# Kernel optimization log

Hardware: AMD Instinct MI355X
Metric: run time of the kernel (lower is better)

The kernel has to match this reference:

```python
import jax, jax.numpy as jnp
import numpy as np

N = 100_000            # particles
E = 3_200_000          # edges (avg degree 32)
DIM = 3
H = 1.0                # kernel_radius
SIGMA = 3.0 / 359.0 / np.pi / H**3   # 3D quintic kernel normalization
RHO_REF = 1.0
P_REF = 100.0          # rho_ref * (10*u_ref)**2 / gamma, gamma=1
P_BG = 0.0             # p_bg_factor * p_ref
ETA0 = 0.01            # base_viscosity
EPS = 1e-8


def _qpows(d, p):
    q = d / H
    return (jnp.maximum(0.0, 1.0 - q) ** p,
            jnp.maximum(0.0, 2.0 - q) ** p,
            jnp.maximum(0.0, 3.0 - q) ** p)


def kernel_w(d):
    q1, q2, q3 = _qpows(d, 5)
    return SIGMA * (q3 - 6.0 * q2 + 15.0 * q1)


def kernel_grad_w(d):
    q1, q2, q3 = _qpows(d, 4)
    return (SIGMA / H) * (-5.0 * q3 + 30.0 * q2 - 75.0 * q1)


def setup_inputs() -> dict:
    key = jax.random.key(0)
    k1, k2, k3, k4 = jax.random.split(key, 4)
    r = jax.random.uniform(k1, (N, DIM), dtype=jnp.float32)   # positions in unit box
    v = jax.random.normal(k2, (N, DIM), dtype=jnp.float32)    # velocity history (last frame)
    i_s = jax.random.randint(k3, (E,), 0, N)                  # receivers
    j_s = jax.random.randint(k4, (E,), 0, N)                  # senders
    return {"r": r, "v": v, "i_s": i_s, "j_s": j_s}


def reference(r, v, i_s, j_s):
    n = r.shape[0]
    # --- per-edge gather + kernel ---
    dr = r[i_s] - r[j_s]                       # displacement_fn, [E,3]
    d = jnp.sqrt(jnp.sum(dr * dr, axis=-1))    # [E]
    w = kernel_w(d)
    # --- density summation (scatter) ---
    mass = jnp.ones((n,), r.dtype)
    rho = mass * jax.ops.segment_sum(w, i_s, num_segments=n)
    # Tait EoS, gamma=1
    p = P_REF * (rho / RHO_REF - 1.0) + P_BG
    eta = jnp.full((n,), ETA0, r.dtype)

    # --- per-edge acceleration (gather particle fields to edges) ---
    rho_i, rho_j = rho[i_s], rho[j_s]
    p_i, p_j = p[i_s], p[j_s]
    eta_i, eta_j = eta[i_s], eta[j_s]
    u_i, u_j = v[i_s], v[j_s]                  # u == v in _transform
    v_i, v_j = u_i, u_j

    eta_ij = 2.0 * eta_i * eta_j / (eta_i + eta_j + EPS)
    p_ij = (rho_j * p_i + rho_i * p_j) / (rho_i + rho_j)
    # ((m_i/rho_i)^2 + (m_j/rho_j)^2)/m_i with m == 1
    wvol = (1.0 / rho_i) ** 2 + (1.0 / rho_j) ** 2
    c = wvol * kernel_grad_w(d) / (d + EPS)    # [E]

    # transport stress A = (outer(rho_i*u_i, v_i-u_i) + outer(rho_j*u_j, v_j-u_j))/2, [E,3,3]
    A = 0.5 * (rho_i[:, None, None] * u_i[:, :, None] * (v_i - u_i)[:, None, :]
               + rho_j[:, None, None] * u_j[:, :, None] * (v_j - u_j)[:, None, :])
    Ar = jnp.einsum('eij,ej->ei', A, dr)

    a_eq_8 = c[:, None] * (-p_ij[:, None] * dr + Ar + eta_ij[:, None] * (u_i - u_j))
    p_bg_i = jnp.zeros_like(p_i)               # _transform passes zeros
    a_eq_13 = (c * p_bg_i)[:, None] * dr

    # --- scatter-reduce to particles ---
    dudt = jax.ops.segment_sum(a_eq_8, i_s, num_segments=n)   # [N,3]
    dvdt = jax.ops.segment_sum(a_eq_13, i_s, num_segments=n)  # [N,3]

    # pack state outputs: [rho, p, dudt(3), dvdt(3)] -> [N,8]
    return jnp.concatenate([rho[:, None], p[:, None], dudt, dvdt], axis=1)
```

## Files before the change

kernel.cpp:

```cpp
#include <hip/hip_runtime.h>
#include <math.h>

#ifndef M_PI
#define M_PI 3.14159265358979323846
#endif

static constexpr float kSigma = (float)(3.0 / 359.0 / M_PI);
static constexpr float kPRef  = 100.0f;
static constexpr float kEps   = 1e-8f;
static constexpr float kEta   = (float)(2.0 * 0.01 * 0.01 / (0.01 + 0.01 + 1e-8));

#define CHUNKH 4096
#define CHUNKS 8192
#define NSUB   8

__device__ __forceinline__ float pow5f(float t) { float t2 = t * t; return t2 * t2 * t; }
__device__ __forceinline__ float pow4f(float t) { float t2 = t * t; return t2 * t2; }

__global__ void k_pack(const float* __restrict__ r, float4* __restrict__ pos4, int n) {
    int i = blockIdx.x * blockDim.x + threadIdx.x;
    if (i >= n) return;
    pos4[i] = make_float4(r[3 * i], r[3 * i + 1], r[3 * i + 2], 0.f);
}

__global__ void k_hist(const int* __restrict__ i_s, int* __restrict__ ghist,
                       int nbAh, int nbins, int E, int shift) {
    __shared__ int h[512];
    int t = threadIdx.x, blk = blockIdx.x;
    for (int b = t; b < nbins; b += 256) h[b] = 0;
    __syncthreads();
    int base = blk * CHUNKH;
    int end = min(base + CHUNKH, E);
    for (int k = base + t; k < end; k += 256)
        atomicAdd(&h[i_s[k] >> shift], 1);
    __syncthreads();
    for (int b = t; b < nbins; b += 256)
        ghist[b * nbAh + blk] = h[b];
}

__global__ void k_scan_block(const int* __restrict__ in, int* __restrict__ out,
                             int* __restrict__ bsum, int m) {
    __shared__ int s[256];
    int t = threadIdx.x;
    int i = blockIdx.x * 256 + t;
    int x = (i < m) ? in[i] : 0;
    s[t] = x;
    __syncthreads();
    for (int d = 1; d < 256; d <<= 1) {
        int v = (t >= d) ? s[t - d] : 0;
        __syncthreads();
        s[t] += v;
        __syncthreads();
    }
    if (i < m) out[i] = s[t] - x;
    if (t == 255) bsum[blockIdx.x] = s[255];
}

__global__ void k_scan_bsums(const int* __restrict__ bsum, int* __restrict__ bscan, int nb) {
    __shared__ int s[512];
    __shared__ int carry;
    int t = threadIdx.x;
    if (t == 0) carry = 0;
    __syncthreads();
    for (int base = 0; base < nb; base += 512) {
        int i = base + t;
        int x = (i < nb) ? bsum[i] : 0;
        s[t] = x;
        __syncthreads();
        for (int d = 1; d < 512; d <<= 1) {
            int v = (t >= d) ? s[t - d] : 0;
            __syncthreads();
            s[t] += v;
            __syncthreads();
        }
        if (i < nb) bscan[i] = s[t] - x + carry;
        __syncthreads();
        if (t == 511) carry += s[511];
        __syncthreads();
    }
}

__device__ __forceinline__ int scanned(const int* __restrict__ gscan,
                                       const int* __restrict__ bscan, int idx) {
    return gscan[idx] + bscan[idx >> 8];
}

__global__ void k_split(const int* __restrict__ i_s, const int* __restrict__ j_s,
                        const int* __restrict__ gscan, const int* __restrict__ bscan,
                        int* __restrict__ pairs, int nbAh, int nbins, int E,
                        int shift, int jbits) {
    __shared__ int cur[512];
    int t = threadIdx.x, blk = blockIdx.x;
    for (int b = t; b < nbins; b += 512)
        cur[b] = scanned(gscan, bscan, b * nbAh + 2 * blk);
    __syncthreads();
    int fmask = (1 << shift) - 1;
    int base = blk * CHUNKS;
    int end = min(base + CHUNKS, E);
    for (int k = base + t; k < end; k += 512) {
        int i = i_s[k];
        int pos = atomicAdd(&cur[i >> shift], 1);
        pairs[pos] = ((i & fmask) << jbits) | j_s[k];
    }
}

__global__ void k_rho_bin(const float4* __restrict__ pos4, const int* __restrict__ pairs,
                          const int* __restrict__ gscan, const int* __restrict__ bscan,
                          float* __restrict__ part_rho, int nbAh, int n, int E,
                          int shift, int jbits, int nbins) {
    __shared__ float srho[256];
    __shared__ float4 spos[256];
    __shared__ int sse[2];
    int bin = blockIdx.x >> 3, sub = blockIdx.x & (NSUB - 1);
    int t = threadIdx.x;
    int lo = bin << shift;
    srho[t] = 0.f;
    int ii = lo + t;
    spos[t] = (ii < n) ? pos4[ii] : make_float4(0.f, 0.f, 0.f, 0.f);
    if (t == 0) {
        sse[0] = scanned(gscan, bscan, bin * nbAh);
        sse[1] = (bin + 1 < nbins) ? scanned(gscan, bscan, (bin + 1) * nbAh) : E;
    }
    __syncthreads();
    int s = sse[0], len = sse[1] - sse[0];
    int k0 = s + (int)((long)len * sub / NSUB);
    int k1 = s + (int)((long)len * (sub + 1) / NSUB);
    int jm = (1 << jbits) - 1;
    for (int k = k0 + t; k < k1; k += 256) {
        int pr = pairs[k];
        int slot = pr >> jbits, j = pr & jm;
        float4 rj = pos4[j];
        float4 ri = spos[slot];
        float dx = ri.x - rj.x, dy = ri.y - rj.y, dz = ri.z - rj.z;
        float d = sqrtf(dx * dx + dy * dy + dz * dz);
        float t1 = fmaxf(1.f - d, 0.f);
        float t2 = fmaxf(2.f - d, 0.f);
        float t3 = fmaxf(3.f - d, 0.f);
        float w = kSigma * (pow5f(t3) - 6.f * pow5f(t2) + 15.f * pow5f(t1));
        atomicAdd(&srho[slot], w);
    }
    __syncthreads();
    if (ii < n) part_rho[(size_t)sub * n + ii] = srho[t];
}

__global__ void k_reduce_rho(const float* __restrict__ part_rho,
                             const float4* __restrict__ pos4, const float* __restrict__ v,
                             float4* __restrict__ pv8, float* __restrict__ out, int n) {
    int i = blockIdx.x * blockDim.x + threadIdx.x;
    if (i >= n) return;
    float rh = 0.f;
    for (int s = 0; s < NSUB; s++) rh += part_rho[(size_t)s * n + i];
    float pp = kPRef * (rh - 1.0f);
    float4 sp = pos4[i];
    pv8[2 * i]     = make_float4(sp.x, sp.y, sp.z, rh);
    pv8[2 * i + 1] = make_float4(v[3 * i], v[3 * i + 1], v[3 * i + 2], pp);
    float* o = out + (size_t)i * 8;
    o[0] = rh;
    o[1] = pp;
    o[5] = 0.f; o[6] = 0.f; o[7] = 0.f;
}

__global__ void k_acc_bin(const float4* __restrict__ pv8, const int* __restrict__ pairs,
                          const int* __restrict__ gscan, const int* __restrict__ bscan,
                          float* __restrict__ part_ax, float* __restrict__ part_ay,
                          float* __restrict__ part_az, int nbAh, int n, int E,
                          int shift, int jbits, int nbins) {
    __shared__ float sax[256], say[256], saz[256];
    __shared__ float4 sab[512];
    __shared__ int sse[2];
    int bin = blockIdx.x >> 3, sub = blockIdx.x & (NSUB - 1);
    int t = threadIdx.x;
    int lo = bin << shift;
    sax[t] = 0.f; say[t] = 0.f; saz[t] = 0.f;
    for (int q = t; q < 512; q += 256) {
        int gi = 2 * lo + q;
        sab[q] = (gi < 2 * n) ? pv8[gi] : make_float4(1.f, 1.f, 1.f, 1.f);
    }
    if (t == 0) {
        sse[0] = scanned(gscan, bscan, bin * nbAh);
        sse[1] = (bin + 1 < nbins) ? scanned(gscan, bscan, (bin + 1) * nbAh) : E;
    }
    __syncthreads();
    int s = sse[0], len = sse[1] - sse[0];
    int k0 = s + (int)((long)len * sub / NSUB);
    int k1 = s + (int)((long)len * (sub + 1) / NSUB);
    int jm = (1 << jbits) - 1;
    for (int k = k0 + t; k < k1; k += 256) {
        int pr = pairs[k];
        int slot = pr >> jbits, j = pr & jm;
        float4 aj = pv8[2 * j];
        float4 bj = pv8[2 * j + 1];
        float4 ai = sab[2 * slot];
        float4 bi = sab[2 * slot + 1];
        float rho_i = ai.w, p_i = bi.w;
        float rho_j = aj.w, p_j = bj.w;
        float dx = ai.x - aj.x, dy = ai.y - aj.y, dz = ai.z - aj.z;
        float d = sqrtf(dx * dx + dy * dy + dz * dz);
        float t1 = fmaxf(1.f - d, 0.f);
        float t2 = fmaxf(2.f - d, 0.f);
        float t3 = fmaxf(3.f - d, 0.f);
        float gw = kSigma * (-5.f * pow4f(t3) + 30.f * pow4f(t2) - 75.f * pow4f(t1));
        float inv_i = 1.0f / rho_i, inv_j = 1.0f / rho_j;
        float c = (inv_i * inv_i + inv_j * inv_j) * gw / (d + kEps);
        float p_ij = (rho_j * p_i + rho_i * p_j) / (rho_i + rho_j);
        atomicAdd(&sax[slot], c * (kEta * (bi.x - bj.x) - p_ij * dx));
        atomicAdd(&say[slot], c * (kEta * (bi.y - bj.y) - p_ij * dy));
        atomicAdd(&saz[slot], c * (kEta * (bi.z - bj.z) - p_ij * dz));
    }
    __syncthreads();
    int ii = lo + t;
    if (ii < n) {
        size_t o = (size_t)sub * n + ii;
        part_ax[o] = sax[t];
        part_ay[o] = say[t];
        part_az[o] = saz[t];
    }
}

__global__ void k_reduce_acc(const float* __restrict__ part_ax,
                             const float* __restrict__ part_ay,
                             const float* __restrict__ part_az,
                             float* __restrict__ out, int n) {
    int i = blockIdx.x * blockDim.x + threadIdx.x;
    if (i >= n) return;
    float ax = 0.f, ay = 0.f, az = 0.f;
    for (int s = 0; s < NSUB; s++) {
        size_t o = (size_t)s * n + i;
        ax += part_ax[o]; ay += part_ay[o]; az += part_az[o];
    }
    float* o = out + (size_t)i * 8 + 2;
    o[0] = ax; o[1] = ay; o[2] = az;
}

static inline char* wcarve(char*& ws, size_t bytes) {
    char* p = ws;
    ws += (bytes + 255) & ~(size_t)255;
    return p;
}

extern "C" void kernel_launch(void* const* d_in, const int* in_sizes, int n_in,
                              void* d_out, int out_size, void* d_ws, size_t ws_size,
                              hipStream_t stream) {
    const float* r = (const float*)d_in[0];
    const float* v = (const float*)d_in[1];
    const int* i_s = (const int*)d_in[2];
    const int* j_s = (const int*)d_in[3];
    int n = in_sizes[0] / 3;
    int E = in_sizes[2];
    float* out = (float*)d_out;

    int shift = 8;
    int nbins = ((n - 1) >> shift) + 1;
    while (nbins > 512) { shift++; nbins = ((n - 1) >> shift) + 1; }
    int jbits = 1;
    while ((1 << jbits) < n) jbits++;

    int nbAh = (E + CHUNKH - 1) / CHUNKH;
    int nbAs = (E + CHUNKS - 1) / CHUNKS;
    int m = nbins * nbAh;
    int nb2 = (m + 255) / 256;

    char* ws = (char*)d_ws;
    float4* pos4    = (float4*)wcarve(ws, (size_t)n * 16);
    float4* pv8     = (float4*)wcarve(ws, (size_t)n * 32);
    int*    ghist   = (int*)wcarve(ws, (size_t)m * 4);
    int*    gscan   = (int*)wcarve(ws, (size_t)m * 4);
    int*    bsum    = (int*)wcarve(ws, (size_t)nb2 * 4);
    int*    bscan   = (int*)wcarve(ws, (size_t)nb2 * 4);
    int*    pairs   = (int*)wcarve(ws, (size_t)E * 4);
    float*  part_rho= (float*)wcarve(ws, (size_t)NSUB * n * 4);
    float*  part_ax = (float*)wcarve(ws, (size_t)NSUB * n * 4);
    float*  part_ay = (float*)wcarve(ws, (size_t)NSUB * n * 4);
    float*  part_az = (float*)wcarve(ws, (size_t)NSUB * n * 4);

    const int bs = 256;
    int gn = (n + bs - 1) / bs;

    k_pack<<<gn, bs, 0, stream>>>(r, pos4, n);
    k_hist<<<nbAh, 256, 0, stream>>>(i_s, ghist, nbAh, nbins, E, shift);
    k_scan_block<<<nb2, 256, 0, stream>>>(ghist, gscan, bsum, m);
    k_scan_bsums<<<1, 512, 0, stream>>>(bsum, bscan, nb2);
    k_split<<<nbAs, 512, 0, stream>>>(i_s, j_s, gscan, bscan, pairs, nbAh, nbins, E, shift, jbits);
    k_rho_bin<<<nbins * NSUB, 256, 0, stream>>>(pos4, pairs, gscan, bscan, part_rho, nbAh, n, E, shift, jbits, nbins);
    k_reduce_rho<<<gn, bs, 0, stream>>>(part_rho, pos4, v, pv8, out, n);
    k_acc_bin<<<nbins * NSUB, 256, 0, stream>>>(pv8, pairs, gscan, bscan, part_ax, part_ay, part_az, nbAh, n, E, shift, jbits, nbins);
    k_reduce_acc<<<gn, bs, 0, stream>>>(part_ax, part_ay, part_az, out, n);
}
```

Measured before the change: 210.9 us.

## Batch gathers for memory-level parallelism and halve sub-splits per bin

The hist, split, rho and acceleration kernels now load several edges' indices and gathered neighbour data into registers before computing, so more independent global loads are in flight per thread. NSUB drops from 8 to 4 and the bin kernels loop over up to 512 slots, so fewer partial buffers have to be written and reduced. The three acceleration partial arrays are merged into one float4 array for vector stores and loads. The batching raises register pressure and may lower occupancy, and with NSUB at 4 there are fewer blocks to fill the GPU.

```diff
diff --git a/kernel.cpp b/kernel.cpp
--- a/kernel.cpp
+++ b/kernel.cpp
@@ -12,7 +12,8 @@
 
 #define CHUNKH 4096
 #define CHUNKS 8192
-#define NSUB   8
+#define NSUB   4
+#define BAT    8
 
 __device__ __forceinline__ float pow5f(float t) { float t2 = t * t; return t2 * t2 * t; }
 __device__ __forceinline__ float pow4f(float t) { float t2 = t * t; return t2 * t2; }
@@ -31,8 +32,17 @@
     __syncthreads();
     int base = blk * CHUNKH;
     int end = min(base + CHUNKH, E);
-    for (int k = base + t; k < end; k += 256)
-        atomicAdd(&h[i_s[k] >> shift], 1);
+    for (int kb = base; kb < end; kb += 256 * 4) {
+        int iv[4];
+#pragma unroll
+        for (int b = 0; b < 4; b++) {
+            int k = kb + b * 256 + t;
+            iv[b] = (k < end) ? i_s[k] : -1;
+        }
+#pragma unroll
+        for (int b = 0; b < 4; b++)
+            if (iv[b] >= 0) atomicAdd(&h[iv[b] >> shift], 1);
+    }
     __syncthreads();
     for (int b = t; b < nbins; b += 256)
         ghist[b * nbAh + blk] = h[b];
@@ -97,10 +107,20 @@
     int fmask = (1 << shift) - 1;
     int base = blk * CHUNKS;
     int end = min(base + CHUNKS, E);
-    for (int k = base + t; k < end; k += 512) {
-        int i = i_s[k];
-        int pos = atomicAdd(&cur[i >> shift], 1);
-        pairs[pos] = ((i & fmask) << jbits) | j_s[k];
+    for (int kb = base; kb < end; kb += 512 * 4) {
+        int iv[4], jv[4];
+#pragma unroll
+        for (int b = 0; b < 4; b++) {
+            int k = kb + b * 512 + t;
+            iv[b] = (k < end) ? i_s[k] : -1;
+            jv[b] = (k < end) ? j_s[k] : 0;
+        }
+#pragma unroll
+        for (int b = 0; b < 4; b++) {
+            if (iv[b] < 0) continue;
+            int pos = atomicAdd(&cur[iv[b] >> shift], 1);
+            pairs[pos] = ((iv[b] & fmask) << jbits) | jv[b];
+        }
     }
 }
 
@@ -108,15 +128,18 @@
                           const int* __restrict__ gscan, const int* __restrict__ bscan,
                           float* __restrict__ part_rho, int nbAh, int n, int E,
                           int shift, int jbits, int nbins) {
-    __shared__ float srho[256];
-    __shared__ float4 spos[256];
+    __shared__ float srho[512];
+    __shared__ float4 spos[512];
     __shared__ int sse[2];
-    int bin = blockIdx.x >> 3, sub = blockIdx.x & (NSUB - 1);
+    int bin = blockIdx.x >> 2, sub = blockIdx.x & (NSUB - 1);
     int t = threadIdx.x;
+    int slots = 1 << shift;
     int lo = bin << shift;
-    srho[t] = 0.f;
-    int ii = lo + t;
-    spos[t] = (ii < n) ? pos4[ii] : make_float4(0.f, 0.f, 0.f, 0.f);
+    for (int s0 = t; s0 < slots; s0 += 256) {
+        srho[s0] = 0.f;
+        int ii = lo + s0;
+        spos[s0] = (ii < n) ? pos4[ii] : make_float4(0.f, 0.f, 0.f, 0.f);
+    }
     if (t == 0) {
         sse[0] = scanned(gscan, bscan, bin * nbAh);
         sse[1] = (bin + 1 < nbins) ? scanned(gscan, bscan, (bin + 1) * nbAh) : E;
@@ -126,21 +149,36 @@
     int k0 = s + (int)((long)len * sub / NSUB);
     int k1 = s + (int)((long)len * (sub + 1) / NSUB);
     int jm = (1 << jbits) - 1;
-    for (int k = k0 + t; k < k1; k += 256) {
-        int pr = pairs[k];
-        int slot = pr >> jbits, j = pr & jm;
-        float4 rj = pos4[j];
-        float4 ri = spos[slot];
-        float dx = ri.x - rj.x, dy = ri.y - rj.y, dz = ri.z - rj.z;
-        float d = sqrtf(dx * dx + dy * dy + dz * dz);
-        float t1 = fmaxf(1.f - d, 0.f);
-        float t2 = fmaxf(2.f - d, 0.f);
-        float t3 = fmaxf(3.f - d, 0.f);
-        float w = kSigma * (pow5f(t3) - 6.f * pow5f(t2) + 15.f * pow5f(t1));
-        atomicAdd(&srho[slot], w);
-    }
-    __syncthreads();
-    if (ii < n) part_rho[(size_t)sub * n + ii] = srho[t];
+    for (int kb = k0; kb < k1; kb += 256 * BAT) {
+        int pr[BAT];
+#pragma unroll
+        for (int b = 0; b < BAT; b++) {
+            int k = kb + b * 256 + t;
+            pr[b] = (k < k1) ? pairs[k] : -1;
+        }
+        float4 rj[BAT];
+#pragma unroll
+        for (int b = 0; b < BAT; b++)
+            if (pr[b] >= 0) rj[b] = pos4[pr[b] & jm];
+#pragma unroll
+        for (int b = 0; b < BAT; b++) {
+            if (pr[b] < 0) continue;
+            int slot = pr[b] >> jbits;
+            float4 ri = spos[slot];
+            float dx = ri.x - rj[b].x, dy = ri.y - rj[b].y, dz = ri.z - rj[b].z;
+            float d = sqrtf(dx * dx + dy * dy + dz * dz);
+            float t1 = fmaxf(1.f - d, 0.f);
+            float t2 = fmaxf(2.f - d, 0.f);
+            float t3 = fmaxf(3.f - d, 0.f);
+            float w = kSigma * (pow5f(t3) - 6.f * pow5f(t2) + 15.f * pow5f(t1));
+            atomicAdd(&srho[slot], w);
+        }
+    }
+    __syncthreads();
+    for (int s0 = t; s0 < slots; s0 += 256) {
+        int ii = lo + s0;
+        if (ii < n) part_rho[(size_t)sub * n + ii] = srho[s0];
+    }
 }
 
 __global__ void k_reduce_rho(const float* __restrict__ part_rho,
@@ -162,17 +200,17 @@
 
 __global__ void k_acc_bin(const float4* __restrict__ pv8, const int* __restrict__ pairs,
                           const int* __restrict__ gscan, const int* __restrict__ bscan,
-                          float* __restrict__ part_ax, float* __restrict__ part_ay,
-                          float* __restrict__ part_az, int nbAh, int n, int E,
+                          float4* __restrict__ part_acc4, int nbAh, int n, int E,
                           int shift, int jbits, int nbins) {
-    __shared__ float sax[256], say[256], saz[256];
-    __shared__ float4 sab[512];
+    __shared__ float sax[512], say[512], saz[512];
+    __shared__ float4 sab[1024];
     __shared__ int sse[2];
-    int bin = blockIdx.x >> 3, sub = blockIdx.x & (NSUB - 1);
+    int bin = blockIdx.x >> 2, sub = blockIdx.x & (NSUB - 1);
     int t = threadIdx.x;
+    int slots = 1 << shift;
     int lo = bin << shift;
-    sax[t] = 0.f; say[t] = 0.f; saz[t] = 0.f;
-    for (int q = t; q < 512; q += 256) {
+    for (int s0 = t; s0 < slots; s0 += 256) { sax[s0] = 0.f; say[s0] = 0.f; saz[s0] = 0.f; }
+    for (int q = t; q < 2 * slots; q += 256) {
         int gi = 2 * lo + q;
         sab[q] = (gi < 2 * n) ? pv8[gi] : make_float4(1.f, 1.f, 1.f, 1.f);
     }
@@ -185,48 +223,60 @@
     int k0 = s + (int)((long)len * sub / NSUB);
     int k1 = s + (int)((long)len * (sub + 1) / NSUB);
     int jm = (1 << jbits) - 1;
-    for (int k = k0 + t; k < k1; k += 256) {
-        int pr = pairs[k];
-        int slot = pr >> jbits, j = pr & jm;
-        float4 aj = pv8[2 * j];
-        float4 bj = pv8[2 * j + 1];
-        float4 ai = sab[2 * slot];
-        float4 bi = sab[2 * slot + 1];
-        float rho_i = ai.w, p_i = bi.w;
-        float rho_j = aj.w, p_j = bj.w;
-        float dx = ai.x - aj.x, dy = ai.y - aj.y, dz = ai.z - aj.z;
-        float d = sqrtf(dx * dx + dy * dy + dz * dz);
-        float t1 = fmaxf(1.f - d, 0.f);
-        float t2 = fmaxf(2.f - d, 0.f);
-        float t3 = fmaxf(3.f - d, 0.f);
-        float gw = kSigma * (-5.f * pow4f(t3) + 30.f * pow4f(t2) - 75.f * pow4f(t1));
-        float inv_i = 1.0f / rho_i, inv_j = 1.0f / rho_j;
-        float c = (inv_i * inv_i + inv_j * inv_j) * gw / (d + kEps);
-        float p_ij = (rho_j * p_i + rho_i * p_j) / (rho_i + rho_j);
-        atomicAdd(&sax[slot], c * (kEta * (bi.x - bj.x) - p_ij * dx));
-        atomicAdd(&say[slot], c * (kEta * (bi.y - bj.y) - p_ij * dy));
-        atomicAdd(&saz[slot], c * (kEta * (bi.z - bj.z) - p_ij * dz));
-    }
-    __syncthreads();
-    int ii = lo + t;
-    if (ii < n) {
-        size_t o = (size_t)sub * n + ii;
-        part_ax[o] = sax[t];
-        part_ay[o] = say[t];
-        part_az[o] = saz[t];
-    }
-}
-
-__global__ void k_reduce_acc(const float* __restrict__ part_ax,
-                             const float* __restrict__ part_ay,
-                             const float* __restrict__ part_az,
+    for (int kb = k0; kb < k1; kb += 256 * BAT) {
+        int pr[BAT];
+#pragma unroll
+        for (int b = 0; b < BAT; b++) {
+            int k = kb + b * 256 + t;
+            pr[b] = (k < k1) ? pairs[k] : -1;
+        }
+        float4 aj[BAT], bj[BAT];
+#pragma unroll
+        for (int b = 0; b < BAT; b++) {
+            if (pr[b] >= 0) {
+                int j = pr[b] & jm;
+                aj[b] = pv8[2 * j];
+                bj[b] = pv8[2 * j + 1];
+            }
+        }
+#pragma unroll
+        for (int b = 0; b < BAT; b++) {
+            if (pr[b] < 0) continue;
+            int slot = pr[b] >> jbits;
+            float4 ai = sab[2 * slot];
+            float4 bi = sab[2 * slot + 1];
+            float rho_i = ai.w, p_i = bi.w;
+            float rho_j = aj[b].w, p_j = bj[b].w;
+            float dx = ai.x - aj[b].x, dy = ai.y - aj[b].y, dz = ai.z - aj[b].z;
+            float d = sqrtf(dx * dx + dy * dy + dz * dz);
+            float t1 = fmaxf(1.f - d, 0.f);
+            float t2 = fmaxf(2.f - d, 0.f);
+            float t3 = fmaxf(3.f - d, 0.f);
+            float gw = kSigma * (-5.f * pow4f(t3) + 30.f * pow4f(t2) - 75.f * pow4f(t1));
+            float inv_i = 1.0f / rho_i, inv_j = 1.0f / rho_j;
+            float c = (inv_i * inv_i + inv_j * inv_j) * gw / (d + kEps);
+            float p_ij = (rho_j * p_i + rho_i * p_j) / (rho_i + rho_j);
+            atomicAdd(&sax[slot], c * (kEta * (bi.x - bj[b].x) - p_ij * dx));
+            atomicAdd(&say[slot], c * (kEta * (bi.y - bj[b].y) - p_ij * dy));
+            atomicAdd(&saz[slot], c * (kEta * (bi.z - bj[b].z) - p_ij * dz));
+        }
+    }
+    __syncthreads();
+    for (int s0 = t; s0 < slots; s0 += 256) {
+        int ii = lo + s0;
+        if (ii < n)
+            part_acc4[(size_t)sub * n + ii] = make_float4(sax[s0], say[s0], saz[s0], 0.f);
+    }
+}
+
+__global__ void k_reduce_acc(const float4* __restrict__ part_acc4,
                              float* __restrict__ out, int n) {
     int i = blockIdx.x * blockDim.x + threadIdx.x;
     if (i >= n) return;
     float ax = 0.f, ay = 0.f, az = 0.f;
     for (int s = 0; s < NSUB; s++) {
-        size_t o = (size_t)s * n + i;
-        ax += part_ax[o]; ay += part_ay[o]; az += part_az[o];
+        float4 p = part_acc4[(size_t)s * n + i];
+        ax += p.x; ay += p.y; az += p.z;
     }
     float* o = out + (size_t)i * 8 + 2;
     o[0] = ax; o[1] = ay; o[2] = az;
@@ -261,17 +311,15 @@
     int nb2 = (m + 255) / 256;
 
     char* ws = (char*)d_ws;
-    float4* pos4    = (float4*)wcarve(ws, (size_t)n * 16);
-    float4* pv8     = (float4*)wcarve(ws, (size_t)n * 32);
-    int*    ghist   = (int*)wcarve(ws, (size_t)m * 4);
-    int*    gscan   = (int*)wcarve(ws, (size_t)m * 4);
-    int*    bsum    = (int*)wcarve(ws, (size_t)nb2 * 4);
-    int*    bscan   = (int*)wcarve(ws, (size_t)nb2 * 4);
-    int*    pairs   = (int*)wcarve(ws, (size_t)E * 4);
-    float*  part_rho= (float*)wcarve(ws, (size_t)NSUB * n * 4);
-    float*  part_ax = (float*)wcarve(ws, (size_t)NSUB * n * 4);
-    float*  part_ay = (float*)wcarve(ws, (size_t)NSUB * n * 4);
-    float*  part_az = (float*)wcarve(ws, (size_t)NSUB * n * 4);
+    float4* pos4     = (float4*)wcarve(ws, (size_t)n * 16);
+    float4* pv8      = (float4*)wcarve(ws, (size_t)n * 32);
+    int*    ghist    = (int*)wcarve(ws, (size_t)m * 4);
+    int*    gscan    = (int*)wcarve(ws, (size_t)m * 4);
+    int*    bsum     = (int*)wcarve(ws, (size_t)nb2 * 4);
+    int*    bscan    = (int*)wcarve(ws, (size_t)nb2 * 4);
+    int*    pairs    = (int*)wcarve(ws, (size_t)E * 4);
+    float*  part_rho = (float*)wcarve(ws, (size_t)NSUB * n * 4);
+    float4* part_acc4= (float4*)wcarve(ws, (size_t)NSUB * n * 16);
 
     const int bs = 256;
     int gn = (n + bs - 1) / bs;
@@ -283,6 +331,6 @@
     k_split<<<nbAs, 512, 0, stream>>>(i_s, j_s, gscan, bscan, pairs, nbAh, nbins, E, shift, jbits);
     k_rho_bin<<<nbins * NSUB, 256, 0, stream>>>(pos4, pairs, gscan, bscan, part_rho, nbAh, n, E, shift, jbits, nbins);
     k_reduce_rho<<<gn, bs, 0, stream>>>(part_rho, pos4, v, pv8, out, n);
-    k_acc_bin<<<nbins * NSUB, 256, 0, stream>>>(pv8, pairs, gscan, bscan, part_ax, part_ay, part_az, nbAh, n, E, shift, jbits, nbins);
-    k_reduce_acc<<<gn, bs, 0, stream>>>(part_ax, part_ay, part_az, out, n);
-}
+    k_acc_bin<<<nbins * NSUB, 256, 0, stream>>>(pv8, pairs, gscan, bscan, part_acc4, nbAh, n, E, shift, jbits, nbins);
+    k_reduce_acc<<<gn, bs, 0, stream>>>(part_acc4, out, n);
+}
```

Result: slower. 221.1 us (+4.8%).
